# Kernel tuning notes

Measured on AMD Instinct MI355X. Metric: run time of the kernel, lower is better.

Reference implementation:

```python
import jax, jax.numpy as jnp
import numpy as np

B, SQ, SK, D, H, DH = 4, 1024, 1024, 1024, 16, 64

def setup_inputs() -> dict:
    key = jax.random.key(0)
    ks = jax.random.split(key, 7)
    s = 0.02
    return {
        "input_ids": jax.random.normal(ks[0], (B, SQ, D), jnp.float32),
        "encoder_output": jax.random.normal(ks[1], (B, SK, D), jnp.float32),
        "position_bias": jax.random.normal(ks[2], (1, H, SQ, SK), jnp.float32),
        "Wq": jax.random.normal(ks[3], (D, H * DH), jnp.float32) * s,
        "Wk": jax.random.normal(ks[4], (D, H * DH), jnp.float32) * s,
        "Wv": jax.random.normal(ks[5], (D, H * DH), jnp.float32) * s,
        "Wo": jax.random.normal(ks[6], (H * DH, D), jnp.float32) * s,
    }

def reference(input_ids, encoder_output, position_bias, Wq, Wk, Wv, Wo):
    # bias-free projections (nn.Linear(..., bias=False))
    q = (input_ids @ Wq).reshape(B, SQ, H, DH).transpose(0, 2, 1, 3)      # [B,H,Sq,dh]
    k = (encoder_output @ Wk).reshape(B, SK, H, DH).transpose(0, 2, 1, 3)  # [B,H,Sk,dh]
    v = (encoder_output @ Wv).reshape(B, SK, H, DH).transpose(0, 2, 1, 3)  # [B,H,Sk,dh]
    # T5-style attention: NO 1/sqrt(dh) scaling, additive position bias
    scores = jnp.einsum("bhqd,bhkd->bhqk", q, k) + position_bias          # [B,H,Sq,Sk]
    attn = jax.nn.softmax(scores, axis=-1)
    ctx = jnp.einsum("bhqk,bhkd->bhqd", attn, v)                          # [B,H,Sq,dh]
    ctx = ctx.transpose(0, 2, 1, 3).reshape(B, SQ, H * DH)
    return ctx @ Wo                                                        # [B,Sq,D]
```

## Files before the change

### kernel.cpp

```cpp
#include <hip/hip_runtime.h>

typedef _Float16 f16;
typedef _Float16 f16x4 __attribute__((ext_vector_type(4)));
typedef _Float16 f16x8 __attribute__((ext_vector_type(8)));
typedef float f32x4 __attribute__((ext_vector_type(4)));

#define LOADLDS16(gp, lp)                                                     \
  __builtin_amdgcn_global_load_lds(                                           \
      (const __attribute__((address_space(1))) void*)(gp),                    \
      (__attribute__((address_space(3))) void*)(lp), 16, 0, 0)

__global__ __launch_bounds__(256) void k_cast2(const float* __restrict__ a,
                                               const float* __restrict__ b,
                                               f16* __restrict__ ya,
                                               f16* __restrict__ yb) {
  int i = blockIdx.x * 256 + threadIdx.x;
  const float* x;
  f16* y;
  if (i < 1048576) {
    x = a; y = ya;
  } else {
    x = b; y = yb; i -= 1048576;
  }
  float4 v = reinterpret_cast<const float4*>(x)[i];
  f16x4 o;
  o[0] = (f16)v.x; o[1] = (f16)v.y; o[2] = (f16)v.z; o[3] = (f16)v.w;
  reinterpret_cast<f16x4*>(y)[i] = o;
}

__global__ __launch_bounds__(256) void k_castw_t(
    const float* __restrict__ w0, const float* __restrict__ w1,
    const float* __restrict__ w2, const float* __restrict__ w3,
    f16* __restrict__ o0, f16* __restrict__ o1, f16* __restrict__ o2,
    f16* __restrict__ o3) {
  const float* W;
  f16* O;
  switch (blockIdx.z) {
    case 0: W = w0; O = o0; break;
    case 1: W = w1; O = o1; break;
    case 2: W = w2; O = o2; break;
    default: W = w3; O = o3; break;
  }
  __shared__ f16 T[64][72];
  const int tid = threadIdx.x;
  const int r0 = blockIdx.y * 64, c0 = blockIdx.x * 64;
#pragma unroll
  for (int i = 0; i < 4; ++i) {
    int c = i * 256 + tid;
    int row = c >> 4, col = (c & 15) * 4;
    float4 v = *reinterpret_cast<const float4*>(W + (size_t)(r0 + row) * 1024 + c0 + col);
    T[col + 0][row] = (f16)v.x;
    T[col + 1][row] = (f16)v.y;
    T[col + 2][row] = (f16)v.z;
    T[col + 3][row] = (f16)v.w;
  }
  __syncthreads();
#pragma unroll
  for (int i = 0; i < 2; ++i) {
    int c = i * 256 + tid;
    int cc = c >> 3, ro = (c & 7) * 8;
    f16x8 v;
#pragma unroll
    for (int j = 0; j < 8; ++j) v[j] = T[cc][ro + j];
    *reinterpret_cast<f16x8*>(O + (size_t)(c0 + cc) * 1024 + r0 + ro) = v;
  }
}

__global__ __launch_bounds__(256) void k_gemm_qkv(const f16* __restrict__ Xq,
                                                  const f16* __restrict__ Xkv,
                                                  const f16* __restrict__ Bt,
                                                  f16* __restrict__ outp) {
  __shared__ f16 As[128 * 64];
  __shared__ f16 Bs[128 * 64];
  const int tid = threadIdx.x;
  const int w = tid >> 6, l = tid & 63;
  const int lr = l & 15, lq = l >> 4;
  const int m0 = blockIdx.y * 128, n0 = blockIdx.x * 128;
  const f16* A = (n0 < 1024) ? Xq : Xkv;
  const int wr = (w >> 1) * 64, wc = (w & 1) * 64;
  const int K = 1024;
  f32x4 acc[4][4] = {};
  for (int kt = 0; kt < K; kt += 64) {
#pragma unroll
    for (int i = 0; i < 4; ++i) {
      int c = (i * 4 + w) * 64 + l;
      LOADLDS16(A + (size_t)(m0 + (c >> 3)) * K + kt + (c & 7) * 8,
                As + (size_t)(i * 4 + w) * 512);
      LOADLDS16(Bt + (size_t)(n0 + (c >> 3)) * K + kt + (c & 7) * 8,
                Bs + (size_t)(i * 4 + w) * 512);
    }
    __syncthreads();
#pragma unroll
    for (int kk = 0; kk < 2; ++kk) {
      f16x8 af[4], bf[4];
#pragma unroll
      for (int m = 0; m < 4; ++m)
        af[m] = *reinterpret_cast<const f16x8*>(As + (wr + m * 16 + lr) * 64 + kk * 32 + lq * 8);
#pragma unroll
      for (int n = 0; n < 4; ++n)
        bf[n] = *reinterpret_cast<const f16x8*>(Bs + (wc + n * 16 + lr) * 64 + kk * 32 + lq * 8);
#pragma unroll
      for (int m = 0; m < 4; ++m)
#pragma unroll
        for (int n = 0; n < 4; ++n)
          acc[m][n] = __builtin_amdgcn_mfma_f32_16x16x32_f16(af[m], bf[n], acc[m][n], 0, 0, 0);
    }
    __syncthreads();
  }
#pragma unroll
  for (int m = 0; m < 4; ++m)
#pragma unroll
    for (int n = 0; n < 4; ++n)
#pragma unroll
      for (int r = 0; r < 4; ++r) {
        int row = m0 + wr + m * 16 + lq * 4 + r;
        int col = n0 + wc + n * 16 + lr;
        int b = row >> 10, s = row & 1023;
        int plane = col >> 10, cc = col & 1023;
        int h = cc >> 6, dh = cc & 63;
        outp[(size_t)plane * 4194304 +
             (((size_t)(b * 16 + h)) * 1024 + s) * 64 + dh] = (f16)acc[m][n][r];
      }
}

__global__ __launch_bounds__(256) void k_gemm_o(const f16* __restrict__ A,
                                                const f16* __restrict__ Bt,
                                                float* __restrict__ out, int M,
                                                int N, int K) {
  __shared__ f16 As[64 * 64];
  __shared__ f16 Bs[128 * 64];
  const int tid = threadIdx.x;
  const int w = tid >> 6, l = tid & 63;
  const int lr = l & 15, lq = l >> 4;
  const int m0 = blockIdx.y * 64, n0 = blockIdx.x * 128;
  const int wr = (w >> 1) * 32, wc = (w & 1) * 64;
  f32x4 acc[2][4] = {};
  for (int kt = 0; kt < K; kt += 64) {
#pragma unroll
    for (int i = 0; i < 2; ++i) {
      int c = (i * 4 + w) * 64 + l;
      LOADLDS16(A + (size_t)(m0 + (c >> 3)) * K + kt + (c & 7) * 8,
                As + (size_t)(i * 4 + w) * 512);
    }
#pragma unroll
    for (int i = 0; i < 4; ++i) {
      int c = (i * 4 + w) * 64 + l;
      LOADLDS16(Bt + (size_t)(n0 + (c >> 3)) * K + kt + (c & 7) * 8,
                Bs + (size_t)(i * 4 + w) * 512);
    }
    __syncthreads();
#pragma unroll
    for (int kk = 0; kk < 2; ++kk) {
      f16x8 af[2], bf[4];
#pragma unroll
      for (int m = 0; m < 2; ++m)
        af[m] = *reinterpret_cast<const f16x8*>(As + (wr + m * 16 + lr) * 64 + kk * 32 + lq * 8);
#pragma unroll
      for (int n = 0; n < 4; ++n)
        bf[n] = *reinterpret_cast<const f16x8*>(Bs + (wc + n * 16 + lr) * 64 + kk * 32 + lq * 8);
#pragma unroll
      for (int m = 0; m < 2; ++m)
#pragma unroll
        for (int n = 0; n < 4; ++n)
          acc[m][n] = __builtin_amdgcn_mfma_f32_16x16x32_f16(af[m], bf[n], acc[m][n], 0, 0, 0);
    }
    __syncthreads();
  }
#pragma unroll
  for (int m = 0; m < 2; ++m)
#pragma unroll
    for (int n = 0; n < 4; ++n)
#pragma unroll
      for (int r = 0; r < 4; ++r) {
        int row = m0 + wr + m * 16 + lq * 4 + r;
        int col = n0 + wc + n * 16 + lr;
        out[(size_t)row * N + col] = acc[m][n][r];
      }
}

__global__ __launch_bounds__(256) void k_vtrans(const f16* __restrict__ vb,
                                                f16* __restrict__ vtb) {
  const int bh = blockIdx.y, s0 = blockIdx.x * 64;
  __shared__ f16 T[64][72];
  const int tid = threadIdx.x;
  const f16* src = vb + (size_t)bh * 1024 * 64;
#pragma unroll
  for (int i = 0; i < 2; ++i) {
    int c = i * 256 + tid;
    int row = c >> 3, co = (c & 7) * 8;
    f16x8 v = *reinterpret_cast<const f16x8*>(src + (size_t)(s0 + row) * 64 + co);
#pragma unroll
    for (int j = 0; j < 8; ++j) T[co + j][row] = v[j];
  }
  __syncthreads();
  f16* dst = vtb + (size_t)bh * 64 * 1024;
#pragma unroll
  for (int i = 0; i < 2; ++i) {
    int c = i * 256 + tid;
    int dh = c >> 3, so = (c & 7) * 8;
    f16x8 v;
#pragma unroll
    for (int j = 0; j < 8; ++j) v[j] = T[dh][so + j];
    *reinterpret_cast<f16x8*>(dst + (size_t)dh * 1024 + s0 + so) = v;
  }
}

__global__ __launch_bounds__(256) void k_attn(const f16* __restrict__ qb,
                                              const f16* __restrict__ kb,
                                              const f16* __restrict__ vtb,
                                              const float* __restrict__ bias,
                                              f16* __restrict__ ctx) {
  const int bid = blockIdx.x;
  const int ord = (bid & 7) * 128 + (bid >> 3);
  const int h = ord >> 6, qt = (ord >> 2) & 15, b = ord & 3;
  const int bh = b * 16 + h;
  const int q0 = qt * 64;
  const int tid = threadIdx.x, w = tid >> 6, l = tid & 63;
  const int lr = l & 15, lq = l >> 4;

  __shared__ f16 Kb[2][2048];
  __shared__ f16 Vb[2][2048];
  __shared__ float Bbf[2][2048];
  __shared__ f16 Ps[4][640];

  const f16* qp = qb + ((size_t)bh * 1024 + q0 + w * 16 + lr) * 64 + lq * 8;
  f16x8 qf0 = *reinterpret_cast<const f16x8*>(qp);
  f16x8 qf1 = *reinterpret_cast<const f16x8*>(qp + 32);

  f32x4 O[4] = {};
  float mrun = -3.0e38f, rsum = 0.f;

  const f16* kbase = kb + (size_t)bh * 1024 * 64;
  const f16* vbase = vtb + (size_t)bh * 64 * 1024;
  const float* bbase = bias + ((size_t)h * 1024 + q0) * 1024;

  const int krow = w * 8 + (l >> 3);
  const int kg = (l & 7) ^ (l >> 3);
  const int vrow = w * 16 + (l >> 2);
  const int vg = (l & 3) ^ ((l >> 3) & 3);
  const int brow = w * 16 + (l >> 3);
  const int bgs = (l & 7) ^ ((l >> 3) & 7);

  auto stage = [&](int t, int nxt) {
    LOADLDS16(kbase + (size_t)(t * 32 + krow) * 64 + kg * 8, &Kb[nxt][w * 512]);
    LOADLDS16(vbase + (size_t)vrow * 1024 + t * 32 + vg * 8, &Vb[nxt][w * 512]);
    LOADLDS16(bbase + (size_t)brow * 1024 + t * 32 + bgs * 4, &Bbf[nxt][w * 512]);
    LOADLDS16(bbase + (size_t)(brow + 8) * 1024 + t * 32 + bgs * 4,
              &Bbf[nxt][w * 512 + 256]);
  };

  stage(0, 0);
  __syncthreads();

#pragma unroll 1
  for (int t = 0; t < 32; ++t) {
    const int cur = t & 1;
    if (t < 31) stage(t + 1, cur ^ 1);
    __builtin_amdgcn_sched_barrier(0);

    f32x4 S[2];
#pragma unroll
    for (int c = 0; c < 2; ++c) {
      int G = c * 4 + lq;
      S[c] = *reinterpret_cast<const f32x4*>(
          &Bbf[cur][(w * 16 + lr) * 32 + ((G ^ (lr & 7)) << 2)]);
    }

    __builtin_amdgcn_s_setprio(1);
#pragma unroll
    for (int c = 0; c < 2; ++c) {
      int row = c * 16 + lr;
      const f16* kbp = &Kb[cur][row * 64];
      f16x8 kf0 = *reinterpret_cast<const f16x8*>(kbp + ((lq ^ (lr & 7)) * 8));
      f16x8 kf1 = *reinterpret_cast<const f16x8*>(kbp + (((4 + lq) ^ (lr & 7)) * 8));
      S[c] = __builtin_amdgcn_mfma_f32_16x16x32_f16(kf0, qf0, S[c], 0, 0, 0);
      S[c] = __builtin_amdgcn_mfma_f32_16x16x32_f16(kf1, qf1, S[c], 0, 0, 0);
    }
    __builtin_amdgcn_s_setprio(0);

    float tmax = fmaxf(fmaxf(fmaxf(S[0][0], S[0][1]), fmaxf(S[0][2], S[0][3])),
                       fmaxf(fmaxf(S[1][0], S[1][1]), fmaxf(S[1][2], S[1][3])));
    if (!__all(tmax <= mrun + 8.0f)) {
      tmax = fmaxf(tmax, __shfl_xor(tmax, 16, 64));
      tmax = fmaxf(tmax, __shfl_xor(tmax, 32, 64));
      float mnew = fmaxf(mrun, tmax);
      float sc = __expf(mrun - mnew);
      mrun = mnew;
      rsum *= sc;
      int sb = l & 48;
#pragma unroll
      for (int r = 0; r < 4; ++r) {
        float scO = __shfl(sc, sb | (lq * 4 + r), 64);
#pragma unroll
        for (int c = 0; c < 4; ++c) O[c][r] *= scO;
      }
    }

#pragma unroll
    for (int c = 0; c < 2; ++c) {
      f32x4 p;
#pragma unroll
      for (int r = 0; r < 4; ++r) p[r] = __expf(S[c][r] - mrun);
      rsum += (p[0] + p[1]) + (p[2] + p[3]);
      f16x4 ph = {(f16)p[0], (f16)p[1], (f16)p[2], (f16)p[3]};
      *reinterpret_cast<f16x4*>(&Ps[w][lr * 40 + c * 16 + lq * 4]) = ph;
    }

    {
      f16x8 pa = *reinterpret_cast<const f16x8*>(&Ps[w][lr * 40 + lq * 8]);
      __builtin_amdgcn_s_setprio(1);
#pragma unroll
      for (int c = 0; c < 4; ++c) {
        int row = c * 16 + lr;
        f16x8 vf = *reinterpret_cast<const f16x8*>(
            &Vb[cur][row * 32 + ((lq ^ ((lr >> 1) & 3)) * 8)]);
        O[c] = __builtin_amdgcn_mfma_f32_16x16x32_f16(pa, vf, O[c], 0, 0, 0);
      }
      __builtin_amdgcn_s_setprio(0);
    }

    __syncthreads();
  }

  rsum += __shfl_xor(rsum, 16, 64);
  rsum += __shfl_xor(rsum, 32, 64);
  int sb = l & 48;
  float rs[4];
#pragma unroll
  for (int r = 0; r < 4; ++r) rs[r] = __shfl(rsum, sb | (lq * 4 + r), 64);

#pragma unroll
  for (int c = 0; c < 4; ++c)
#pragma unroll
    for (int r = 0; r < 4; ++r) {
      float o = O[c][r] / rs[r];
      int row = q0 + w * 16 + lq * 4 + r;
      ctx[((size_t)b * 1024 + row) * 1024 + h * 64 + c * 16 + lr] = (f16)o;
    }
}

extern "C" void kernel_launch(void* const* d_in, const int* in_sizes, int n_in,
                              void* d_out, int out_size, void* d_ws,
                              size_t ws_size, hipStream_t stream) {
  const float* input_ids = (const float*)d_in[0];
  const float* enc = (const float*)d_in[1];
  const float* bias = (const float*)d_in[2];
  const float* Wq = (const float*)d_in[3];
  const float* Wk = (const float*)d_in[4];
  const float* Wv = (const float*)d_in[5];
  const float* Wo = (const float*)d_in[6];

  char* ws = (char*)d_ws;
  const size_t MB = 1024 * 1024;
  f16* Xq  = (f16*)(ws + 0 * MB);
  f16* Xkv = (f16*)(ws + 8 * MB);
  f16* Wqt = (f16*)(ws + 16 * MB);
  f16* Wkt = (f16*)(ws + 18 * MB);
  f16* Wvt = (f16*)(ws + 20 * MB);
  f16* Wot = (f16*)(ws + 22 * MB);
  f16* qbuf = (f16*)(ws + 24 * MB);
  f16* kbuf = (f16*)(ws + 32 * MB);
  f16* vbuf = (f16*)(ws + 40 * MB);
  f16* vtb = Xkv;
  f16* ctxb = Xq;

  k_cast2<<<8192, 256, 0, stream>>>(input_ids, enc, Xq, Xkv);
  k_castw_t<<<dim3(16, 16, 4), 256, 0, stream>>>(Wq, Wk, Wv, Wo, Wqt, Wkt, Wvt, Wot);

  k_gemm_qkv<<<dim3(24, 32), 256, 0, stream>>>(Xq, Xkv, Wqt, qbuf);

  k_vtrans<<<dim3(16, 64), 256, 0, stream>>>(vbuf, vtb);

  k_attn<<<1024, 256, 0, stream>>>(qbuf, kbuf, vtb, bias, ctxb);

  k_gemm_o<<<dim3(8, 64), 256, 0, stream>>>(ctxb, Wot, (float*)d_out, 4096, 1024, 1024);
}
```

Measured before the change: 140.1 us.

## Double attention query tile per wave and triple-buffer K/V with one barrier

Each wave now handles 32 query rows (two 16-row fragments) instead of 16, so every K/V fragment read from LDS feeds two MFMAs. The workgroup count drops from 1024 to 512. The pipeline changes from double buffering to a 3-stage K/V ring plus a double-buffered bias tile, using explicit vmcnt waits and a single barrier per iteration instead of the trailing __syncthreads. This is meant to cut LDS traffic and barrier stalls per unit of work, at the cost of more registers and LDS per block, fewer blocks, and hand-written waitcnt logic that relies on the order loads are issued.

```diff
diff --git a/kernel.cpp b/kernel.cpp
--- a/kernel.cpp
+++ b/kernel.cpp
@@ -205,138 +205,179 @@
   }
 }
 
-__global__ __launch_bounds__(256) void k_attn(const f16* __restrict__ qb,
-                                              const f16* __restrict__ kb,
-                                              const f16* __restrict__ vtb,
-                                              const float* __restrict__ bias,
-                                              f16* __restrict__ ctx) {
+__global__ __launch_bounds__(256, 2) void k_attn(const f16* __restrict__ qb,
+                                                 const f16* __restrict__ kb,
+                                                 const f16* __restrict__ vtb,
+                                                 const float* __restrict__ bias,
+                                                 f16* __restrict__ ctx) {
   const int bid = blockIdx.x;
-  const int ord = (bid & 7) * 128 + (bid >> 3);
-  const int h = ord >> 6, qt = (ord >> 2) & 15, b = ord & 3;
+  const int ord = (bid & 7) * 64 + (bid >> 3);
+  const int h = ord >> 5, qt = (ord >> 2) & 7, b = ord & 3;
   const int bh = b * 16 + h;
-  const int q0 = qt * 64;
+  const int q0 = qt * 128;
   const int tid = threadIdx.x, w = tid >> 6, l = tid & 63;
   const int lr = l & 15, lq = l >> 4;
 
-  __shared__ f16 Kb[2][2048];
-  __shared__ f16 Vb[2][2048];
-  __shared__ float Bbf[2][2048];
-  __shared__ f16 Ps[4][640];
-
-  const f16* qp = qb + ((size_t)bh * 1024 + q0 + w * 16 + lr) * 64 + lq * 8;
-  f16x8 qf0 = *reinterpret_cast<const f16x8*>(qp);
-  f16x8 qf1 = *reinterpret_cast<const f16x8*>(qp + 32);
-
-  f32x4 O[4] = {};
-  float mrun = -3.0e38f, rsum = 0.f;
-
-  const f16* kbase = kb + (size_t)bh * 1024 * 64;
-  const f16* vbase = vtb + (size_t)bh * 64 * 1024;
+  __shared__ f16 Kb3[3][2048];
+  __shared__ f16 Vb3[3][2048];
+  __shared__ float Bb2[2][4096];
+  __shared__ f16 Ps[4][1280];
+
+  const f16* qp = qb + ((size_t)bh * 1024 + q0 + w * 32 + lr) * 64 + lq * 8;
+  f16x8 qA0 = *reinterpret_cast<const f16x8*>(qp);
+  f16x8 qA1 = *reinterpret_cast<const f16x8*>(qp + 32);
+  f16x8 qB0 = *reinterpret_cast<const f16x8*>(qp + 1024);
+  f16x8 qB1 = *reinterpret_cast<const f16x8*>(qp + 1056);
+
+  f32x4 OA[4] = {}, OB[4] = {};
+  float mA = -3.0e38f, mB = -3.0e38f, rsA = 0.f, rsB = 0.f;
+
+  const f16* kbase = kb + (size_t)bh * 65536;
+  const f16* vbase = vtb + (size_t)bh * 65536;
   const float* bbase = bias + ((size_t)h * 1024 + q0) * 1024;
 
-  const int krow = w * 8 + (l >> 3);
-  const int kg = (l & 7) ^ (l >> 3);
-  const int vrow = w * 16 + (l >> 2);
-  const int vg = (l & 3) ^ ((l >> 3) & 3);
-  const int brow = w * 16 + (l >> 3);
-  const int bgs = (l & 7) ^ ((l >> 3) & 7);
-
-  auto stage = [&](int t, int nxt) {
-    LOADLDS16(kbase + (size_t)(t * 32 + krow) * 64 + kg * 8, &Kb[nxt][w * 512]);
-    LOADLDS16(vbase + (size_t)vrow * 1024 + t * 32 + vg * 8, &Vb[nxt][w * 512]);
-    LOADLDS16(bbase + (size_t)brow * 1024 + t * 32 + bgs * 4, &Bbf[nxt][w * 512]);
-    LOADLDS16(bbase + (size_t)(brow + 8) * 1024 + t * 32 + bgs * 4,
-              &Bbf[nxt][w * 512 + 256]);
+  const int krow = w * 8 + (l >> 3), kg = (l & 7) ^ (l >> 3);
+  const int vrow = w * 16 + (l >> 2), vg = (l & 3) ^ ((l >> 3) & 3);
+
+  auto stage_kv = [&](int t, int c3) {
+    LOADLDS16(kbase + (size_t)(t * 32 + krow) * 64 + kg * 8, &Kb3[c3][w * 512]);
+    LOADLDS16(vbase + (size_t)vrow * 1024 + t * 32 + vg * 8, &Vb3[c3][w * 512]);
   };
-
-  stage(0, 0);
-  __syncthreads();
+  auto stage_b = [&](int t, int c2) {
+#pragma unroll
+    for (int j = 0; j < 4; ++j) {
+      int c4 = w * 4 + j;
+      int row = c4 * 8 + (l >> 3);
+      int gs = (l & 7) ^ (l >> 3);
+      LOADLDS16(bbase + (size_t)row * 1024 + t * 32 + gs * 4,
+                &Bb2[c2][c4 * 256]);
+    }
+  };
+
+  stage_b(0, 0);
+  stage_kv(0, 0);
+  stage_kv(1, 1);
 
 #pragma unroll 1
   for (int t = 0; t < 32; ++t) {
-    const int cur = t & 1;
-    if (t < 31) stage(t + 1, cur ^ 1);
+    if (t < 31) {
+      asm volatile("s_waitcnt vmcnt(2)" ::: "memory");
+    } else {
+      asm volatile("s_waitcnt vmcnt(0)" ::: "memory");
+    }
+    __builtin_amdgcn_s_barrier();
     __builtin_amdgcn_sched_barrier(0);
 
-    f32x4 S[2];
-#pragma unroll
-    for (int c = 0; c < 2; ++c) {
-      int G = c * 4 + lq;
-      S[c] = *reinterpret_cast<const f32x4*>(
-          &Bbf[cur][(w * 16 + lr) * 32 + ((G ^ (lr & 7)) << 2)]);
-    }
+    if (t + 1 < 32) stage_b(t + 1, (t + 1) & 1);
+    if (t + 2 < 32) stage_kv(t + 2, (t + 2) % 3);
+    __builtin_amdgcn_sched_barrier(0);
+
+    const int c3 = t % 3, c2 = t & 1;
+    const f16* Kc = &Kb3[c3][0];
+    const f16* Vc = &Vb3[c3][0];
+    const float* Bc = &Bb2[c2][0];
+
+    f32x4 S[2][2];
+#pragma unroll
+    for (int f = 0; f < 2; ++f)
+#pragma unroll
+      for (int c = 0; c < 2; ++c) {
+        int row = w * 32 + f * 16 + lr;
+        int pos = (c * 4 + lq) ^ (lr & 7);
+        S[f][c] = *reinterpret_cast<const f32x4*>(&Bc[row * 32 + pos * 4]);
+      }
 
     __builtin_amdgcn_s_setprio(1);
 #pragma unroll
     for (int c = 0; c < 2; ++c) {
       int row = c * 16 + lr;
-      const f16* kbp = &Kb[cur][row * 64];
+      const f16* kbp = &Kc[row * 64];
       f16x8 kf0 = *reinterpret_cast<const f16x8*>(kbp + ((lq ^ (lr & 7)) * 8));
       f16x8 kf1 = *reinterpret_cast<const f16x8*>(kbp + (((4 + lq) ^ (lr & 7)) * 8));
-      S[c] = __builtin_amdgcn_mfma_f32_16x16x32_f16(kf0, qf0, S[c], 0, 0, 0);
-      S[c] = __builtin_amdgcn_mfma_f32_16x16x32_f16(kf1, qf1, S[c], 0, 0, 0);
+      S[0][c] = __builtin_amdgcn_mfma_f32_16x16x32_f16(kf0, qA0, S[0][c], 0, 0, 0);
+      S[0][c] = __builtin_amdgcn_mfma_f32_16x16x32_f16(kf1, qA1, S[0][c], 0, 0, 0);
+      S[1][c] = __builtin_amdgcn_mfma_f32_16x16x32_f16(kf0, qB0, S[1][c], 0, 0, 0);
+      S[1][c] = __builtin_amdgcn_mfma_f32_16x16x32_f16(kf1, qB1, S[1][c], 0, 0, 0);
     }
     __builtin_amdgcn_s_setprio(0);
 
-    float tmax = fmaxf(fmaxf(fmaxf(S[0][0], S[0][1]), fmaxf(S[0][2], S[0][3])),
-                       fmaxf(fmaxf(S[1][0], S[1][1]), fmaxf(S[1][2], S[1][3])));
-    if (!__all(tmax <= mrun + 8.0f)) {
-      tmax = fmaxf(tmax, __shfl_xor(tmax, 16, 64));
-      tmax = fmaxf(tmax, __shfl_xor(tmax, 32, 64));
-      float mnew = fmaxf(mrun, tmax);
-      float sc = __expf(mrun - mnew);
-      mrun = mnew;
-      rsum *= sc;
+    float tA = fmaxf(fmaxf(fmaxf(S[0][0][0], S[0][0][1]), fmaxf(S[0][0][2], S[0][0][3])),
+                     fmaxf(fmaxf(S[0][1][0], S[0][1][1]), fmaxf(S[0][1][2], S[0][1][3])));
+    float tB = fmaxf(fmaxf(fmaxf(S[1][0][0], S[1][0][1]), fmaxf(S[1][0][2], S[1][0][3])),
+                     fmaxf(fmaxf(S[1][1][0], S[1][1][1]), fmaxf(S[1][1][2], S[1][1][3])));
+    bool ok = (tA <= mA + 8.0f) && (tB <= mB + 8.0f);
+    if (!__all(ok)) {
+      tA = fmaxf(tA, __shfl_xor(tA, 16, 64));
+      tA = fmaxf(tA, __shfl_xor(tA, 32, 64));
+      tB = fmaxf(tB, __shfl_xor(tB, 16, 64));
+      tB = fmaxf(tB, __shfl_xor(tB, 32, 64));
+      float mnA = fmaxf(mA, tA), mnB = fmaxf(mB, tB);
+      float scA = __expf(mA - mnA), scB = __expf(mB - mnB);
+      mA = mnA; mB = mnB;
+      rsA *= scA; rsB *= scB;
       int sb = l & 48;
 #pragma unroll
       for (int r = 0; r < 4; ++r) {
-        float scO = __shfl(sc, sb | (lq * 4 + r), 64);
-#pragma unroll
-        for (int c = 0; c < 4; ++c) O[c][r] *= scO;
+        float sA = __shfl(scA, sb | (lq * 4 + r), 64);
+        float sB = __shfl(scB, sb | (lq * 4 + r), 64);
+#pragma unroll
+        for (int c = 0; c < 4; ++c) {
+          OA[c][r] *= sA;
+          OB[c][r] *= sB;
+        }
       }
     }
 
 #pragma unroll
     for (int c = 0; c < 2; ++c) {
-      f32x4 p;
-#pragma unroll
-      for (int r = 0; r < 4; ++r) p[r] = __expf(S[c][r] - mrun);
-      rsum += (p[0] + p[1]) + (p[2] + p[3]);
-      f16x4 ph = {(f16)p[0], (f16)p[1], (f16)p[2], (f16)p[3]};
-      *reinterpret_cast<f16x4*>(&Ps[w][lr * 40 + c * 16 + lq * 4]) = ph;
+      f32x4 pA, pB;
+#pragma unroll
+      for (int r = 0; r < 4; ++r) {
+        pA[r] = __expf(S[0][c][r] - mA);
+        pB[r] = __expf(S[1][c][r] - mB);
+      }
+      rsA += (pA[0] + pA[1]) + (pA[2] + pA[3]);
+      rsB += (pB[0] + pB[1]) + (pB[2] + pB[3]);
+      f16x4 hA = {(f16)pA[0], (f16)pA[1], (f16)pA[2], (f16)pA[3]};
+      f16x4 hB = {(f16)pB[0], (f16)pB[1], (f16)pB[2], (f16)pB[3]};
+      *reinterpret_cast<f16x4*>(&Ps[w][lr * 40 + c * 16 + lq * 4]) = hA;
+      *reinterpret_cast<f16x4*>(&Ps[w][(16 + lr) * 40 + c * 16 + lq * 4]) = hB;
     }
 
     {
-      f16x8 pa = *reinterpret_cast<const f16x8*>(&Ps[w][lr * 40 + lq * 8]);
+      f16x8 paA = *reinterpret_cast<const f16x8*>(&Ps[w][lr * 40 + lq * 8]);
+      f16x8 paB = *reinterpret_cast<const f16x8*>(&Ps[w][(16 + lr) * 40 + lq * 8]);
       __builtin_amdgcn_s_setprio(1);
 #pragma unroll
       for (int c = 0; c < 4; ++c) {
         int row = c * 16 + lr;
         f16x8 vf = *reinterpret_cast<const f16x8*>(
-            &Vb[cur][row * 32 + ((lq ^ ((lr >> 1) & 3)) * 8)]);
-        O[c] = __builtin_amdgcn_mfma_f32_16x16x32_f16(pa, vf, O[c], 0, 0, 0);
+            &Vc[row * 32 + ((lq ^ ((lr >> 1) & 3)) * 8)]);
+        OA[c] = __builtin_amdgcn_mfma_f32_16x16x32_f16(paA, vf, OA[c], 0, 0, 0);
+        OB[c] = __builtin_amdgcn_mfma_f32_16x16x32_f16(paB, vf, OB[c], 0, 0, 0);
       }
       __builtin_amdgcn_s_setprio(0);
     }
-
-    __syncthreads();
-  }
-
-  rsum += __shfl_xor(rsum, 16, 64);
-  rsum += __shfl_xor(rsum, 32, 64);
+  }
+
+  rsA += __shfl_xor(rsA, 16, 64);
+  rsA += __shfl_xor(rsA, 32, 64);
+  rsB += __shfl_xor(rsB, 16, 64);
+  rsB += __shfl_xor(rsB, 32, 64);
   int sb = l & 48;
-  float rs[4];
-#pragma unroll
-  for (int r = 0; r < 4; ++r) rs[r] = __shfl(rsum, sb | (lq * 4 + r), 64);
-
-#pragma unroll
-  for (int c = 0; c < 4; ++c)
-#pragma unroll
-    for (int r = 0; r < 4; ++r) {
-      float o = O[c][r] / rs[r];
-      int row = q0 + w * 16 + lq * 4 + r;
-      ctx[((size_t)b * 1024 + row) * 1024 + h * 64 + c * 16 + lr] = (f16)o;
-    }
+
+#pragma unroll
+  for (int r = 0; r < 4; ++r) {
+    float dA = __shfl(rsA, sb | (lq * 4 + r), 64);
+    float dB = __shfl(rsB, sb | (lq * 4 + r), 64);
+    int rowA = q0 + w * 32 + lq * 4 + r;
+#pragma unroll
+    for (int c = 0; c < 4; ++c) {
+      int col = h * 64 + c * 16 + lr;
+      ctx[((size_t)b * 1024 + rowA) * 1024 + col] = (f16)(OA[c][r] / dA);
+      ctx[((size_t)b * 1024 + rowA + 16) * 1024 + col] = (f16)(OB[c][r] / dB);
+    }
+  }
 }
 
 extern "C" void kernel_launch(void* const* d_in, const int* in_sizes, int n_in,
@@ -371,7 +412,7 @@
 
   k_vtrans<<<dim3(16, 64), 256, 0, stream>>>(vbuf, vtb);
 
-  k_attn<<<1024, 256, 0, stream>>>(qbuf, kbuf, vtb, bias, ctxb);
+  k_attn<<<512, 256, 0, stream>>>(qbuf, kbuf, vtb, bias, ctxb);
 
   k_gemm_o<<<dim3(8, 64), 256, 0, stream>>>(ctxb, Wot, (float*)d_out, 4096, 1024, 1024);
 }
```

New measurement: 140.3 us. No clear change (+0.2%).

## Double KV tile to 64 keys and load position bias directly into registers

Applied to the files above, without the earlier changes.

The attention loop now processes 64 keys per iteration instead of 32, which halves the iteration count and the number of block barriers. The position bias is no longer staged through shared memory with async LDS loads; each lane reads its own f32x4 bias fragments straight from global memory into registers and adds them after the QK MFMAs. K and V shared buffers double in size while the bias buffer is dropped. The direct bias loads rely on the sched barrier and MFMA work to hide latency, and larger tiles raise register pressure.

```diff
diff --git a/kernel.cpp b/kernel.cpp
--- a/kernel.cpp
+++ b/kernel.cpp
@@ -218,9 +218,8 @@
   const int tid = threadIdx.x, w = tid >> 6, l = tid & 63;
   const int lr = l & 15, lq = l >> 4;
 
-  __shared__ f16 Kb[2][2048];
-  __shared__ f16 Vb[2][2048];
-  __shared__ float Bbf[2][2048];
+  __shared__ f16 Kb[2][4096];
+  __shared__ f16 Vb[2][4096];
   __shared__ f16 Ps[4][640];
 
   const f16* qp = qb + ((size_t)bh * 1024 + q0 + w * 16 + lr) * 64 + lq * 8;
@@ -230,56 +229,58 @@
   f32x4 O[4] = {};
   float mrun = -3.0e38f, rsum = 0.f;
 
-  const f16* kbase = kb + (size_t)bh * 1024 * 64;
-  const f16* vbase = vtb + (size_t)bh * 64 * 1024;
-  const float* bbase = bias + ((size_t)h * 1024 + q0) * 1024;
-
-  const int krow = w * 8 + (l >> 3);
-  const int kg = (l & 7) ^ (l >> 3);
-  const int vrow = w * 16 + (l >> 2);
-  const int vg = (l & 3) ^ ((l >> 3) & 3);
-  const int brow = w * 16 + (l >> 3);
-  const int bgs = (l & 7) ^ ((l >> 3) & 7);
+  const f16* kbase = kb + (size_t)bh * 65536;
+  const f16* vbase = vtb + (size_t)bh * 65536;
+  const float* bq = bias + ((size_t)h * 1024 + q0 + w * 16 + lr) * 1024 + lq * 4;
 
   auto stage = [&](int t, int nxt) {
-    LOADLDS16(kbase + (size_t)(t * 32 + krow) * 64 + kg * 8, &Kb[nxt][w * 512]);
-    LOADLDS16(vbase + (size_t)vrow * 1024 + t * 32 + vg * 8, &Vb[nxt][w * 512]);
-    LOADLDS16(bbase + (size_t)brow * 1024 + t * 32 + bgs * 4, &Bbf[nxt][w * 512]);
-    LOADLDS16(bbase + (size_t)(brow + 8) * 1024 + t * 32 + bgs * 4,
-              &Bbf[nxt][w * 512 + 256]);
+#pragma unroll
+    for (int i = 0; i < 2; ++i) {
+      int c = (i * 4 + w) * 64 + l;
+      int row = c >> 3, g = (c & 7) ^ (row & 7);
+      LOADLDS16(kbase + (size_t)(t * 64 + row) * 64 + g * 8,
+                &Kb[nxt][(i * 4 + w) * 512]);
+      LOADLDS16(vbase + (size_t)row * 1024 + t * 64 + g * 8,
+                &Vb[nxt][(i * 4 + w) * 512]);
+    }
   };
 
   stage(0, 0);
   __syncthreads();
 
 #pragma unroll 1
-  for (int t = 0; t < 32; ++t) {
+  for (int t = 0; t < 16; ++t) {
     const int cur = t & 1;
-    if (t < 31) stage(t + 1, cur ^ 1);
+    if (t < 15) stage(t + 1, cur ^ 1);
+    f32x4 bf[4];
+#pragma unroll
+    for (int c = 0; c < 4; ++c)
+      bf[c] = *reinterpret_cast<const f32x4*>(bq + t * 64 + c * 16);
     __builtin_amdgcn_sched_barrier(0);
 
-    f32x4 S[2];
-#pragma unroll
-    for (int c = 0; c < 2; ++c) {
-      int G = c * 4 + lq;
-      S[c] = *reinterpret_cast<const f32x4*>(
-          &Bbf[cur][(w * 16 + lr) * 32 + ((G ^ (lr & 7)) << 2)]);
-    }
-
+    f32x4 S[4] = {};
     __builtin_amdgcn_s_setprio(1);
 #pragma unroll
-    for (int c = 0; c < 2; ++c) {
+    for (int c = 0; c < 4; ++c) {
       int row = c * 16 + lr;
       const f16* kbp = &Kb[cur][row * 64];
-      f16x8 kf0 = *reinterpret_cast<const f16x8*>(kbp + ((lq ^ (lr & 7)) * 8));
-      f16x8 kf1 = *reinterpret_cast<const f16x8*>(kbp + (((4 + lq) ^ (lr & 7)) * 8));
+      f16x8 kf0 = *reinterpret_cast<const f16x8*>(kbp + ((lq ^ (row & 7)) * 8));
+      f16x8 kf1 = *reinterpret_cast<const f16x8*>(kbp + (((4 + lq) ^ (row & 7)) * 8));
       S[c] = __builtin_amdgcn_mfma_f32_16x16x32_f16(kf0, qf0, S[c], 0, 0, 0);
       S[c] = __builtin_amdgcn_mfma_f32_16x16x32_f16(kf1, qf1, S[c], 0, 0, 0);
     }
     __builtin_amdgcn_s_setprio(0);
 
-    float tmax = fmaxf(fmaxf(fmaxf(S[0][0], S[0][1]), fmaxf(S[0][2], S[0][3])),
-                       fmaxf(fmaxf(S[1][0], S[1][1]), fmaxf(S[1][2], S[1][3])));
+#pragma unroll
+    for (int c = 0; c < 4; ++c)
+#pragma unroll
+      for (int r = 0; r < 4; ++r) S[c][r] += bf[c][r];
+
+    float tmax = fmaxf(
+        fmaxf(fmaxf(fmaxf(S[0][0], S[0][1]), fmaxf(S[0][2], S[0][3])),
+              fmaxf(fmaxf(S[1][0], S[1][1]), fmaxf(S[1][2], S[1][3]))),
+        fmaxf(fmaxf(fmaxf(S[2][0], S[2][1]), fmaxf(S[2][2], S[2][3])),
+              fmaxf(fmaxf(S[3][0], S[3][1]), fmaxf(S[3][2], S[3][3]))));
     if (!__all(tmax <= mrun + 8.0f)) {
       tmax = fmaxf(tmax, __shfl_xor(tmax, 16, 64));
       tmax = fmaxf(tmax, __shfl_xor(tmax, 32, 64));
@@ -305,19 +306,30 @@
       f16x4 ph = {(f16)p[0], (f16)p[1], (f16)p[2], (f16)p[3]};
       *reinterpret_cast<f16x4*>(&Ps[w][lr * 40 + c * 16 + lq * 4]) = ph;
     }
-
-    {
-      f16x8 pa = *reinterpret_cast<const f16x8*>(&Ps[w][lr * 40 + lq * 8]);
-      __builtin_amdgcn_s_setprio(1);
-#pragma unroll
-      for (int c = 0; c < 4; ++c) {
-        int row = c * 16 + lr;
-        f16x8 vf = *reinterpret_cast<const f16x8*>(
-            &Vb[cur][row * 32 + ((lq ^ ((lr >> 1) & 3)) * 8)]);
-        O[c] = __builtin_amdgcn_mfma_f32_16x16x32_f16(pa, vf, O[c], 0, 0, 0);
-      }
-      __builtin_amdgcn_s_setprio(0);
-    }
+    f16x8 pa0 = *reinterpret_cast<const f16x8*>(&Ps[w][lr * 40 + lq * 8]);
+
+#pragma unroll
+    for (int c = 2; c < 4; ++c) {
+      f32x4 p;
+#pragma unroll
+      for (int r = 0; r < 4; ++r) p[r] = __expf(S[c][r] - mrun);
+      rsum += (p[0] + p[1]) + (p[2] + p[3]);
+      f16x4 ph = {(f16)p[0], (f16)p[1], (f16)p[2], (f16)p[3]};
+      *reinterpret_cast<f16x4*>(&Ps[w][lr * 40 + (c - 2) * 16 + lq * 4]) = ph;
+    }
+    f16x8 pa1 = *reinterpret_cast<const f16x8*>(&Ps[w][lr * 40 + lq * 8]);
+
+    __builtin_amdgcn_s_setprio(1);
+#pragma unroll
+    for (int c = 0; c < 4; ++c) {
+      int row = c * 16 + lr;
+      const f16* vbp = &Vb[cur][row * 64];
+      f16x8 vf0 = *reinterpret_cast<const f16x8*>(vbp + ((lq ^ (row & 7)) * 8));
+      f16x8 vf1 = *reinterpret_cast<const f16x8*>(vbp + (((4 + lq) ^ (row & 7)) * 8));
+      O[c] = __builtin_amdgcn_mfma_f32_16x16x32_f16(pa0, vf0, O[c], 0, 0, 0);
+      O[c] = __builtin_amdgcn_mfma_f32_16x16x32_f16(pa1, vf1, O[c], 0, 0, 0);
+    }
+    __builtin_amdgcn_s_setprio(0);
 
     __syncthreads();
   }
```

Result: no change. 141.3 us (+0.9%).
